# Kernel tuning notes

Measured on AMD Instinct MI355X. Metric: run time of the kernel, lower is better.

Reference implementation:

```python
import jax, jax.numpy as jnp
import numpy as np

B, L, C, R = 64, 4096, 256, 8
H = C // R  # 32

def setup_inputs() -> dict:
    key = jax.random.key(0)
    k0, k1, k2 = jax.random.split(key, 3)
    inputs = jax.random.normal(k0, (B, L, C), dtype=jnp.float32)
    # Dense weights (glorot-ish scale)
    w1 = jax.random.normal(k1, (C, H), dtype=jnp.float32) * (1.0 / np.sqrt(C))
    b1 = jnp.zeros((H,), dtype=jnp.float32)
    w2 = jax.random.normal(k2, (H, C), dtype=jnp.float32) * (1.0 / np.sqrt(H))
    b2 = jnp.zeros((C,), dtype=jnp.float32)
    return {"inputs": inputs, "w1": w1, "b1": b1, "w2": w2, "b2": b2}

def reference(inputs, w1, b1, w2, b2):
    # squeeze: global average pool over sequence dim -> [B, C]
    s = jnp.mean(inputs, axis=1)
    # excitation: C -> C//R (relu) -> C (sigmoid)
    e = jax.nn.relu(s @ w1 + b1)
    g = jax.nn.sigmoid(e @ w2 + b2)  # [B, C]
    # broadcast gate over sequence dim and scale
    return inputs * g[:, None, :]
```

## Files before the change

### kernel.cpp

```cpp
#include <hip/hip_runtime.h>
#include <math.h>

constexpr int B = 64;
constexpr int L = 4096;
constexpr int C = 256;
constexpr int H = 32;

constexpr int NCH = 32;
constexpr int ROWS = L / NCH;

typedef float v4f __attribute__((ext_vector_type(4)));

__global__ __launch_bounds__(256) void se_reduce(const float* __restrict__ in,
                                                 float* __restrict__ partial) {
    const int b = blockIdx.x / NCH;
    const int chunk = blockIdx.x % NCH;
    const int t = threadIdx.x;
    const int c4 = t & 63;
    const int r0 = t >> 6;

    const v4f* base = reinterpret_cast<const v4f*>(
        in + (size_t)b * L * C + (size_t)chunk * ROWS * C);

    v4f acc = (v4f)(0.f);
    #pragma unroll
    for (int grp = 0; grp < 4; ++grp) {
        const size_t i0 = (size_t)(r0 + grp * 32) * (C / 4) + c4;
        v4f v[8];
        #pragma unroll
        for (int j = 0; j < 8; ++j)
            v[j] = base[i0 + (size_t)j * 4 * (C / 4)];
        #pragma unroll
        for (int j = 0; j < 8; ++j)
            acc += v[j];
    }

    __shared__ v4f red[4][C / 4];
    red[r0][c4] = acc;
    __syncthreads();
    if (r0 == 0) {
        v4f s = red[0][c4] + red[1][c4] + red[2][c4] + red[3][c4];
        reinterpret_cast<v4f*>(partial + (size_t)blockIdx.x * C)[c4] = s;
    }
}

__global__ __launch_bounds__(256) void se_gate_scale(
        const float* __restrict__ partial,
        const float* __restrict__ w1,
        const float* __restrict__ b1,
        const float* __restrict__ w2,
        const float* __restrict__ b2,
        const v4f* __restrict__ in,
        v4f* __restrict__ out) {
    const int b = blockIdx.x / NCH;
    const int chunk = blockIdx.x % NCH;
    const int t = threadIdx.x;
    const int c4 = t & 63;
    const int r0 = t >> 6;

    __shared__ float sm[C];
    __shared__ float em[H];
    __shared__ float gsm[C];

    {
        float acc = 0.f;
        const float* p = partial + (size_t)b * NCH * C + t;
        #pragma unroll 8
        for (int k = 0; k < NCH; ++k) acc += p[(size_t)k * C];
        sm[t] = acc * (1.0f / (float)L);
    }
    __syncthreads();

    if (t < H) {
        float a1 = b1[t];
        #pragma unroll 8
        for (int c = 0; c < C; ++c) a1 += sm[c] * w1[c * H + t];
        em[t] = fmaxf(a1, 0.0f);
    }
    __syncthreads();

    {
        float a2 = b2[t];
        #pragma unroll
        for (int h = 0; h < H; ++h) a2 += em[h] * w2[h * C + t];
        gsm[t] = 1.0f / (1.0f + expf(-a2));
    }
    __syncthreads();

    const v4f gv = *reinterpret_cast<const v4f*>(&gsm[4 * c4]);

    const size_t base = (size_t)b * L * (C / 4)
                      + (size_t)chunk * ROWS * (C / 4) + c4;

    #pragma unroll
    for (int grp = 0; grp < 4; ++grp) {
        const size_t i0 = base + (size_t)(r0 + grp * 32) * (C / 4);
        v4f v[8];
        #pragma unroll
        for (int j = 0; j < 8; ++j)
            v[j] = __builtin_nontemporal_load(&in[i0 + (size_t)j * 4 * (C / 4)]);
        #pragma unroll
        for (int j = 0; j < 8; ++j)
            __builtin_nontemporal_store(v[j] * gv, &out[i0 + (size_t)j * 4 * (C / 4)]);
    }
}

extern "C" void kernel_launch(void* const* d_in, const int* in_sizes, int n_in,
                              void* d_out, int out_size, void* d_ws, size_t ws_size,
                              hipStream_t stream) {
    const float* in = (const float*)d_in[0];
    const float* w1 = (const float*)d_in[1];
    const float* b1 = (const float*)d_in[2];
    const float* w2 = (const float*)d_in[3];
    const float* b2 = (const float*)d_in[4];
    float* out = (float*)d_out;

    float* partial = (float*)d_ws;

    se_reduce<<<B * NCH, 256, 0, stream>>>(in, partial);
    se_gate_scale<<<B * NCH, 256, 0, stream>>>(
        partial, w1, b1, w2, b2,
        reinterpret_cast<const v4f*>(in), reinterpret_cast<v4f*>(out));
}
```

Before: 141.0 us.

## Fuse reduce and gate-scale into one persistent kernel with grid barriers

Merges the two kernels into one persistent kernel of 1024 blocks synchronised by atomic grid barriers. Each block reduces its segment, the first 64 blocks compute the gate (with a parallelised first matvec), and then every block rescales the same segment it just read. The aim is to cut a launch and to reuse the input while it may still be in cache (about 256KB per block, so partly L2/MALL), avoiding redundant per-block gate computation. It risks deadlock if the 1024 blocks are not all co-resident, adds barrier spin cost, and needs an extra memset launch.

```diff
diff --git a/kernel.cpp b/kernel.cpp
--- a/kernel.cpp
+++ b/kernel.cpp
@@ -6,102 +6,111 @@
 constexpr int C = 256;
 constexpr int H = 32;
 
-constexpr int NCH = 32;
-constexpr int ROWS = L / NCH;
+constexpr int NBLK = 1024;
+constexpr int SEGS = NBLK / B;
+constexpr int SROWS = L / SEGS;
 
 typedef float v4f __attribute__((ext_vector_type(4)));
 
-__global__ __launch_bounds__(256) void se_reduce(const float* __restrict__ in,
-                                                 float* __restrict__ partial) {
-    const int b = blockIdx.x / NCH;
-    const int chunk = blockIdx.x % NCH;
+__device__ __forceinline__ void grid_barrier(unsigned int* cnt, unsigned int target) {
+    __syncthreads();
+    if (threadIdx.x == 0) {
+        __threadfence();
+        atomicAdd(cnt, 1u);
+        while (atomicAdd(cnt, 0u) < target) {
+            __builtin_amdgcn_s_sleep(2);
+        }
+    }
+    __syncthreads();
+    __threadfence();
+}
+
+__global__ __launch_bounds__(256, 4) void se_fused(
+        const float* __restrict__ in,
+        const float* __restrict__ w1, const float* __restrict__ b1,
+        const float* __restrict__ w2, const float* __restrict__ b2,
+        v4f* __restrict__ out,
+        float* __restrict__ partial, float* __restrict__ g,
+        unsigned int* __restrict__ bar) {
+    const int j = blockIdx.x;
+    const int b = j >> 4;
+    const int seg = j & 15;
     const int t = threadIdx.x;
     const int c4 = t & 63;
     const int r0 = t >> 6;
 
-    const v4f* base = reinterpret_cast<const v4f*>(
-        in + (size_t)b * L * C + (size_t)chunk * ROWS * C);
+    const v4f* base = reinterpret_cast<const v4f*>(in)
+                    + (size_t)b * L * (C / 4) + (size_t)seg * SROWS * (C / 4);
 
     v4f acc = (v4f)(0.f);
     #pragma unroll
-    for (int grp = 0; grp < 4; ++grp) {
+    for (int grp = 0; grp < 8; ++grp) {
         const size_t i0 = (size_t)(r0 + grp * 32) * (C / 4) + c4;
         v4f v[8];
         #pragma unroll
-        for (int j = 0; j < 8; ++j)
-            v[j] = base[i0 + (size_t)j * 4 * (C / 4)];
+        for (int k = 0; k < 8; ++k) v[k] = base[i0 + (size_t)k * 4 * (C / 4)];
         #pragma unroll
-        for (int j = 0; j < 8; ++j)
-            acc += v[j];
+        for (int k = 0; k < 8; ++k) acc += v[k];
     }
-
     __shared__ v4f red[4][C / 4];
     red[r0][c4] = acc;
     __syncthreads();
     if (r0 == 0) {
         v4f s = red[0][c4] + red[1][c4] + red[2][c4] + red[3][c4];
-        reinterpret_cast<v4f*>(partial + (size_t)blockIdx.x * C)[c4] = s;
+        reinterpret_cast<v4f*>(partial + (size_t)j * C)[c4] = s;
     }
-}
 
-__global__ __launch_bounds__(256) void se_gate_scale(
-        const float* __restrict__ partial,
-        const float* __restrict__ w1,
-        const float* __restrict__ b1,
-        const float* __restrict__ w2,
-        const float* __restrict__ b2,
-        const v4f* __restrict__ in,
-        v4f* __restrict__ out) {
-    const int b = blockIdx.x / NCH;
-    const int chunk = blockIdx.x % NCH;
-    const int t = threadIdx.x;
-    const int c4 = t & 63;
-    const int r0 = t >> 6;
+    grid_barrier(&bar[0], NBLK);
 
-    __shared__ float sm[C];
-    __shared__ float em[H];
-    __shared__ float gsm[C];
+    if (j < B) {
+        __shared__ float sm[C];
+        __shared__ float ep[8][H];
+        __shared__ float em[H];
 
-    {
-        float acc = 0.f;
-        const float* p = partial + (size_t)b * NCH * C + t;
-        #pragma unroll 8
-        for (int k = 0; k < NCH; ++k) acc += p[(size_t)k * C];
-        sm[t] = acc * (1.0f / (float)L);
-    }
-    __syncthreads();
+        float a = 0.f;
+        const float* p = partial + (size_t)j * SEGS * C + t;
+        #pragma unroll
+        for (int k = 0; k < SEGS; ++k) a += p[(size_t)k * C];
+        sm[t] = a * (1.0f / (float)L);
+        __syncthreads();
 
-    if (t < H) {
-        float a1 = b1[t];
-        #pragma unroll 8
-        for (int c = 0; c < C; ++c) a1 += sm[c] * w1[c * H + t];
-        em[t] = fmaxf(a1, 0.0f);
-    }
-    __syncthreads();
+        {
+            const int h = t & 31, cs = t >> 5;
+            float a1 = 0.f;
+            #pragma unroll 8
+            for (int c = cs * 32; c < cs * 32 + 32; ++c) a1 += sm[c] * w1[c * H + h];
+            ep[cs][h] = a1;
+        }
+        __syncthreads();
+        if (t < H) {
+            float a1 = b1[t];
+            #pragma unroll
+            for (int k = 0; k < 8; ++k) a1 += ep[k][t];
+            em[t] = fmaxf(a1, 0.0f);
+        }
+        __syncthreads();
 
-    {
         float a2 = b2[t];
         #pragma unroll
         for (int h = 0; h < H; ++h) a2 += em[h] * w2[h * C + t];
-        gsm[t] = 1.0f / (1.0f + expf(-a2));
+        g[j * C + t] = 1.0f / (1.0f + expf(-a2));
     }
-    __syncthreads();
 
-    const v4f gv = *reinterpret_cast<const v4f*>(&gsm[4 * c4]);
+    grid_barrier(&bar[1], NBLK);
 
-    const size_t base = (size_t)b * L * (C / 4)
-                      + (size_t)chunk * ROWS * (C / 4) + c4;
+    const v4f gv = reinterpret_cast<const v4f*>(g)[b * (C / 4) + c4];
+    v4f* outb = out + (size_t)b * L * (C / 4) + (size_t)seg * SROWS * (C / 4);
 
     #pragma unroll
-    for (int grp = 0; grp < 4; ++grp) {
-        const size_t i0 = base + (size_t)(r0 + grp * 32) * (C / 4);
+    for (int grp = 0; grp < 8; ++grp) {
+        const size_t i0 = (size_t)(r0 + grp * 32) * (C / 4) + c4;
         v4f v[8];
         #pragma unroll
-        for (int j = 0; j < 8; ++j)
-            v[j] = __builtin_nontemporal_load(&in[i0 + (size_t)j * 4 * (C / 4)]);
+        for (int k = 0; k < 8; ++k)
+            v[k] = __builtin_nontemporal_load(&base[i0 + (size_t)k * 4 * (C / 4)]);
         #pragma unroll
-        for (int j = 0; j < 8; ++j)
-            __builtin_nontemporal_store(v[j] * gv, &out[i0 + (size_t)j * 4 * (C / 4)]);
+        for (int k = 0; k < 8; ++k)
+            __builtin_nontemporal_store(v[k] * gv, &outb[i0 + (size_t)k * 4 * (C / 4)]);
     }
 }
 
@@ -113,12 +122,12 @@
     const float* b1 = (const float*)d_in[2];
     const float* w2 = (const float*)d_in[3];
     const float* b2 = (const float*)d_in[4];
-    float* out = (float*)d_out;
+    v4f* out = (v4f*)d_out;
 
     float* partial = (float*)d_ws;
+    float* g = partial + (size_t)NBLK * C;
+    unsigned int* bar = (unsigned int*)(g + B * C);
 
-    se_reduce<<<B * NCH, 256, 0, stream>>>(in, partial);
-    se_gate_scale<<<B * NCH, 256, 0, stream>>>(
-        partial, w1, b1, w2, b2,
-        reinterpret_cast<const v4f*>(in), reinterpret_cast<v4f*>(out));
+    hipMemsetAsync(bar, 0, 2 * sizeof(unsigned int), stream);
+    se_fused<<<NBLK, 256, 0, stream>>>(in, w1, b1, w2, b2, out, partial, g, bar);
 }
```

Measured after the change: 471.0 us. +234.0%, slower.
